# Performance work log

Hardware: AMD Instinct MI355X
Metric: run time of the kernel (lower is better)

Reference implementation:

```python
import jax, jax.numpy as jnp
import numpy as np

NUM_ITERATIONS = 3  # matches init kwarg num_iterations
B, R, CIN, COUT, K = 32, 2048, 64, 64, 16


def squash(s):
    # squash along the last (capsule-vector) axis, as in the torch module
    sq = jnp.sum(s * s, axis=-1, keepdims=True)
    return (sq / (1.0 + sq)) * s / jnp.sqrt(sq)


def setup_inputs() -> dict:
    key = jax.random.key(0)
    k1, k2 = jax.random.split(key)
    x = jax.random.normal(k1, (B, R, CIN), dtype=jnp.float32)
    route_weights = jax.random.normal(k2, (K, R, CIN, COUT), dtype=jnp.float32) * 0.05
    return {"x": x, "route_weights": route_weights}


def reference(x, route_weights):
    # priors[k,b,r,o] = sum_c x[b,r,c] * W[k,r,c,o]   -> [K, B, R, COUT]
    priors = jnp.einsum('brc,krco->kbro', x, route_weights)
    logits = jnp.zeros(priors.shape[:3] + (1,), dtype=priors.dtype)  # [K,B,R,1]
    outputs = None
    for i in range(NUM_ITERATIONS):
        probs = jax.nn.softmax(logits, axis=2)  # softmax over route nodes (torch dim=2)
        outputs = squash(jnp.sum(probs * priors, axis=2, keepdims=True))  # [K,B,1,COUT]
        if i != NUM_ITERATIONS - 1:
            logits = logits + jnp.sum(priors * outputs, axis=-1, keepdims=True)
    return outputs[:, :, 0, :]  # [K, B, COUT]
```

## Files before the change

### kernel.cpp

```cpp
#include <hip/hip_runtime.h>
#include <hip/hip_bf16.h>
#include <stdint.h>

#define NB 32
#define NR 2048
#define NC 64
#define NO 64
#define NK 16

using bf16x8 = __attribute__((ext_vector_type(8))) short;
using f32x4  = __attribute__((ext_vector_type(4))) float;

__device__ __forceinline__ uint32_t f2bf(float f) {
  uint32_t u = __builtin_bit_cast(uint32_t, f);
  return (u + 0x7fffu + ((u >> 16) & 1u)) >> 16;
}
__device__ __forceinline__ uint32_t packbf2(float lo, float hi) {
  return f2bf(lo) | (f2bf(hi) << 16);
}
__device__ __forceinline__ uint32_t cvtpk2(float lo, float hi) {
  float2 v; v.x = lo; v.y = hi;
  __hip_bfloat162 h = __float22bfloat162_rn(v);
  uint32_t r;
  __builtin_memcpy(&r, &h, 4);
  return r;
}

__global__ __launch_bounds__(256) void make_xbf(const float* __restrict__ x,
                                                ushort* __restrict__ xbf) {
  __shared__ float tile[32][72];
  const int r = blockIdx.x, t = threadIdx.x;
  {
    const int b = t >> 3, c0 = (t & 7) << 3;
    const float* xp = x + ((size_t)b * NR + r) * NC + c0;
    *(float4*)&tile[b][c0] = *(const float4*)xp;
    *(float4*)&tile[b][c0 + 4] = *(const float4*)(xp + 4);
  }
  __syncthreads();
  {
    const int ks = t >> 7, bt = (t >> 6) & 1, l = t & 63;
    const int kgrp = l >> 4;
    const int b = bt * 16 + (l & 15);
    const int cb = ks * 32 + kgrp;
    uint4 uv;
    uv.x = packbf2(tile[b][cb + 0], tile[b][cb + 4]);
    uv.y = packbf2(tile[b][cb + 8], tile[b][cb + 12]);
    uv.z = packbf2(tile[b][cb + 16], tile[b][cb + 20]);
    uv.w = packbf2(tile[b][cb + 24], tile[b][cb + 28]);
    *(uint4*)(xbf + (size_t)r * 2048 + t * 8) = uv;
  }
}

__global__ __launch_bounds__(256) void priors_gemm(const ushort* __restrict__ xbf,
                                                   const float* __restrict__ W,
                                                   ushort* __restrict__ priors) {
  __shared__ ushort ldsE[4][32 * 72];
  const int w = threadIdx.x >> 6, lane = threadIdx.x & 63;
  const int kgrp = lane >> 4, col = lane & 15;
  const int task = blockIdx.x * 4 + w;
  const int k = task & 15, r = task >> 4;
  const float* wbase = W + ((size_t)(k * NR + r)) * 4096;
  const ushort* xb = xbf + (size_t)r * 2048;

  bf16x8 xfrag[2][2];
#pragma unroll
  for (int ks = 0; ks < 2; ++ks)
#pragma unroll
    for (int bt = 0; bt < 2; ++bt)
      xfrag[ks][bt] = *(const bf16x8*)(xb + (ks * 2 + bt) * 512 + lane * 8);

  f32x4 acc[4][2];
#pragma unroll
  for (int ot = 0; ot < 4; ++ot)
#pragma unroll
    for (int bt = 0; bt < 2; ++bt) acc[ot][bt] = f32x4{0.f, 0.f, 0.f, 0.f};

#pragma unroll
  for (int ks = 0; ks < 2; ++ks) {
    float w32[4][8];
#pragma unroll
    for (int e = 0; e < 8; ++e) {
      const float* src = wbase + (ks * 32 + e * 4 + kgrp) * 64 + col;
#pragma unroll
      for (int ot = 0; ot < 4; ++ot) w32[ot][e] = src[ot * 16];
    }
#pragma unroll
    for (int ot = 0; ot < 4; ++ot) {
      uint4 uv;
      uv.x = cvtpk2(w32[ot][0], w32[ot][1]);
      uv.y = cvtpk2(w32[ot][2], w32[ot][3]);
      uv.z = cvtpk2(w32[ot][4], w32[ot][5]);
      uv.w = cvtpk2(w32[ot][6], w32[ot][7]);
      bf16x8 af = __builtin_bit_cast(bf16x8, uv);
      acc[ot][0] = __builtin_amdgcn_mfma_f32_16x16x32_bf16(af, xfrag[ks][0], acc[ot][0], 0, 0, 0);
      acc[ot][1] = __builtin_amdgcn_mfma_f32_16x16x32_bf16(af, xfrag[ks][1], acc[ot][1], 0, 0, 0);
    }
  }

  ushort* ep = &ldsE[w][0];
#pragma unroll
  for (int ot = 0; ot < 4; ++ot)
#pragma unroll
    for (int bt = 0; bt < 2; ++bt)
#pragma unroll
      for (int pr = 0; pr < 2; ++pr) {
        uint32_t u = cvtpk2(acc[ot][bt][pr * 2], acc[ot][bt][pr * 2 + 1]);
        const int b = bt * 16 + col, o = ot * 16 + kgrp * 4 + pr * 2;
        *(uint32_t*)(&ep[b * 72 + o]) = u;
      }
  ushort* pp = priors + ((size_t)(k * NR + r)) * 2048;
#pragma unroll
  for (int i = 0; i < 4; ++i) {
    const int row = (lane >> 3) + i * 8, cc = (lane & 7) * 8;
    uint4 v = *(const uint4*)(&ep[row * 72 + cc]);
    *(uint4*)(pp + row * 64 + cc) = v;
  }
}

template <int PASS>
__global__ __launch_bounds__(256) void routing(const __hip_bfloat16* __restrict__ priors,
                                               float* __restrict__ Abuf,
                                               const float* __restrict__ o_prev,
                                               float* __restrict__ o_out) {
  __shared__ float o_lds[64];
  __shared__ float red_num[4][8][8];
  __shared__ float red_den[4];
  const int kb = blockIdx.x;
  const int k = kb >> 5, b = kb & 31;
  const int tid = threadIdx.x, w = tid >> 6, lane = tid & 63;
  const int g = lane >> 3, sl = lane & 7;
  const int rsub = w * 8 + g;
  const __hip_bfloat16* pbase = priors + (size_t)k * NR * NB * NO + (size_t)b * NO;
  float* ab = Abuf + (size_t)kb * NR;

  if (PASS == 1) {
    float sum[8];
#pragma unroll
    for (int j = 0; j < 8; ++j) sum[j] = 0.f;
    for (int it = 0; it < NR / 32; ++it) {
      const int r = it * 32 + rsub;
      uint4 pv = *(const uint4*)(pbase + (size_t)r * (NB * NO) + sl * 8);
      sum[0] += __builtin_bit_cast(float, pv.x << 16);
      sum[1] += __builtin_bit_cast(float, pv.x & 0xffff0000u);
      sum[2] += __builtin_bit_cast(float, pv.y << 16);
      sum[3] += __builtin_bit_cast(float, pv.y & 0xffff0000u);
      sum[4] += __builtin_bit_cast(float, pv.z << 16);
      sum[5] += __builtin_bit_cast(float, pv.z & 0xffff0000u);
      sum[6] += __builtin_bit_cast(float, pv.w << 16);
      sum[7] += __builtin_bit_cast(float, pv.w & 0xffff0000u);
    }
#pragma unroll
    for (int m = 8; m < 64; m <<= 1)
#pragma unroll
      for (int j = 0; j < 8; ++j) sum[j] += __shfl_xor(sum[j], m, 64);
    if (lane < 8) {
#pragma unroll
      for (int j = 0; j < 8; ++j) red_num[w][lane][j] = sum[j];
    }
    __syncthreads();
    if (tid < 64) {
      const int s_ = tid >> 3, j_ = tid & 7;
      float sv = (red_num[0][s_][j_] + red_num[1][s_][j_] +
                  red_num[2][s_][j_] + red_num[3][s_][j_]) * (1.f / (float)NR);
      float sq = sv * sv;
#pragma unroll
      for (int m = 1; m < 64; m <<= 1) sq += __shfl_xor(sq, m, 64);
      o_lds[tid] = (sq / (1.f + sq)) * rsqrtf(sq) * sv;
    }
    __syncthreads();
  } else {
    if (tid < 64) o_lds[tid] = o_prev[kb * 64 + tid];
    __syncthreads();
  }

  float os[8];
#pragma unroll
  for (int j = 0; j < 8; ++j) os[j] = o_lds[sl * 8 + j];

  float num[8];
#pragma unroll
  for (int j = 0; j < 8; ++j) num[j] = 0.f;
  float den = 0.f;

  for (int it = 0; it < NR / 32; ++it) {
    const int r = it * 32 + rsub;
    uint4 pv = *(const uint4*)(pbase + (size_t)r * (NB * NO) + sl * 8);
    float f[8];
    f[0] = __builtin_bit_cast(float, pv.x << 16);
    f[1] = __builtin_bit_cast(float, pv.x & 0xffff0000u);
    f[2] = __builtin_bit_cast(float, pv.y << 16);
    f[3] = __builtin_bit_cast(float, pv.y & 0xffff0000u);
    f[4] = __builtin_bit_cast(float, pv.z << 16);
    f[5] = __builtin_bit_cast(float, pv.z & 0xffff0000u);
    f[6] = __builtin_bit_cast(float, pv.w << 16);
    f[7] = __builtin_bit_cast(float, pv.w & 0xffff0000u);

    float d = 0.f;
#pragma unroll
    for (int j = 0; j < 8; ++j) d = fmaf(f[j], os[j], d);
#pragma unroll
    for (int m = 1; m < 8; m <<= 1) d += __shfl_xor(d, m, 64);

    float lg;
    if (PASS == 1) {
      lg = d;
      if (sl == 0) ab[r] = d;
    } else {
      lg = d + ab[r];
    }
    float e = __expf(lg);
    den += e;
#pragma unroll
    for (int j = 0; j < 8; ++j) num[j] = fmaf(e, f[j], num[j]);
  }

#pragma unroll
  for (int m = 8; m < 64; m <<= 1) {
    den += __shfl_xor(den, m, 64);
#pragma unroll
    for (int j = 0; j < 8; ++j) num[j] += __shfl_xor(num[j], m, 64);
  }
  if (lane < 8) {
#pragma unroll
    for (int j = 0; j < 8; ++j) red_num[w][lane][j] = num[j];
    if (lane == 0) red_den[w] = den;
  }
  __syncthreads();

  if (tid < 64) {
    const int s_ = tid >> 3, j_ = tid & 7;
    float nm = red_num[0][s_][j_] + red_num[1][s_][j_] + red_num[2][s_][j_] + red_num[3][s_][j_];
    float dn = red_den[0] + red_den[1] + red_den[2] + red_den[3];
    float sv = nm / dn;
    float sq = sv * sv;
#pragma unroll
    for (int m = 1; m < 64; m <<= 1) sq += __shfl_xor(sq, m, 64);
    float ov = (sq / (1.f + sq)) * rsqrtf(sq) * sv;
    o_out[kb * 64 + tid] = ov;
  }
}

extern "C" void kernel_launch(void* const* d_in, const int* in_sizes, int n_in,
                              void* d_out, int out_size, void* d_ws, size_t ws_size,
                              hipStream_t stream) {
  const float* x = (const float*)d_in[0];
  const float* W = (const float*)d_in[1];
  float* out = (float*)d_out;
  char* ws = (char*)d_ws;

  size_t off = 0;
  ushort* xbf = (ushort*)(ws + off);               off += (size_t)NR * 2048 * 2;
  ushort* priors = (ushort*)(ws + off);            off += (size_t)NK * NR * NB * NO * 2;
  float* o1 = (float*)(ws + off);                  off += (size_t)NK * NB * NO * 4;
  float* Abuf = (float*)(ws + off);                off += (size_t)NK * NB * NR * 4;

  make_xbf<<<NR, 256, 0, stream>>>(x, xbf);
  priors_gemm<<<(NR * NK) / 4, 256, 0, stream>>>(xbf, W, priors);
  routing<1><<<NK * NB, 256, 0, stream>>>((const __hip_bfloat16*)priors, Abuf, nullptr, o1);
  routing<2><<<NK * NB, 256, 0, stream>>>((const __hip_bfloat16*)priors, Abuf, o1, out);
}
```

Baseline: 219.6 us.

## Fuse two routing passes into one kernel and hoist all W loads in GEMM

```diff
diff --git a/kernel.cpp b/kernel.cpp
--- a/kernel.cpp
+++ b/kernel.cpp
@@ -69,33 +69,35 @@
     for (int bt = 0; bt < 2; ++bt)
       xfrag[ks][bt] = *(const bf16x8*)(xb + (ks * 2 + bt) * 512 + lane * 8);
 
-  f32x4 acc[4][2];
-#pragma unroll
-  for (int ot = 0; ot < 4; ++ot)
-#pragma unroll
-    for (int bt = 0; bt < 2; ++bt) acc[ot][bt] = f32x4{0.f, 0.f, 0.f, 0.f};
-
-#pragma unroll
-  for (int ks = 0; ks < 2; ++ks) {
-    float w32[4][8];
+  float w32[2][4][8];
+#pragma unroll
+  for (int ks = 0; ks < 2; ++ks)
 #pragma unroll
     for (int e = 0; e < 8; ++e) {
       const float* src = wbase + (ks * 32 + e * 4 + kgrp) * 64 + col;
 #pragma unroll
-      for (int ot = 0; ot < 4; ++ot) w32[ot][e] = src[ot * 16];
-    }
+      for (int ot = 0; ot < 4; ++ot) w32[ks][ot][e] = src[ot * 16];
+    }
+
+  f32x4 acc[4][2];
+#pragma unroll
+  for (int ot = 0; ot < 4; ++ot)
+#pragma unroll
+    for (int bt = 0; bt < 2; ++bt) acc[ot][bt] = f32x4{0.f, 0.f, 0.f, 0.f};
+
+#pragma unroll
+  for (int ks = 0; ks < 2; ++ks)
 #pragma unroll
     for (int ot = 0; ot < 4; ++ot) {
       uint4 uv;
-      uv.x = cvtpk2(w32[ot][0], w32[ot][1]);
-      uv.y = cvtpk2(w32[ot][2], w32[ot][3]);
-      uv.z = cvtpk2(w32[ot][4], w32[ot][5]);
-      uv.w = cvtpk2(w32[ot][6], w32[ot][7]);
+      uv.x = cvtpk2(w32[ks][ot][0], w32[ks][ot][1]);
+      uv.y = cvtpk2(w32[ks][ot][2], w32[ks][ot][3]);
+      uv.z = cvtpk2(w32[ks][ot][4], w32[ks][ot][5]);
+      uv.w = cvtpk2(w32[ks][ot][6], w32[ks][ot][7]);
       bf16x8 af = __builtin_bit_cast(bf16x8, uv);
       acc[ot][0] = __builtin_amdgcn_mfma_f32_16x16x32_bf16(af, xfrag[ks][0], acc[ot][0], 0, 0, 0);
       acc[ot][1] = __builtin_amdgcn_mfma_f32_16x16x32_bf16(af, xfrag[ks][1], acc[ot][1], 0, 0, 0);
     }
-  }
 
   ushort* ep = &ldsE[w][0];
 #pragma unroll
@@ -117,23 +119,20 @@
   }
 }
 
-template <int PASS>
-__global__ __launch_bounds__(256) void routing(const __hip_bfloat16* __restrict__ priors,
-                                               float* __restrict__ Abuf,
-                                               const float* __restrict__ o_prev,
-                                               float* __restrict__ o_out) {
+__global__ __launch_bounds__(256) void routing_fused(const __hip_bfloat16* __restrict__ priors,
+                                                     float* __restrict__ o_out) {
   __shared__ float o_lds[64];
   __shared__ float red_num[4][8][8];
   __shared__ float red_den[4];
+  __shared__ float ar[2048];
   const int kb = blockIdx.x;
   const int k = kb >> 5, b = kb & 31;
   const int tid = threadIdx.x, w = tid >> 6, lane = tid & 63;
   const int g = lane >> 3, sl = lane & 7;
   const int rsub = w * 8 + g;
   const __hip_bfloat16* pbase = priors + (size_t)k * NR * NB * NO + (size_t)b * NO;
-  float* ab = Abuf + (size_t)kb * NR;
-
-  if (PASS == 1) {
+
+  {
     float sum[8];
 #pragma unroll
     for (int j = 0; j < 8; ++j) sum[j] = 0.f;
@@ -168,75 +167,77 @@
       o_lds[tid] = (sq / (1.f + sq)) * rsqrtf(sq) * sv;
     }
     __syncthreads();
-  } else {
-    if (tid < 64) o_lds[tid] = o_prev[kb * 64 + tid];
-    __syncthreads();
-  }
-
-  float os[8];
-#pragma unroll
-  for (int j = 0; j < 8; ++j) os[j] = o_lds[sl * 8 + j];
-
-  float num[8];
-#pragma unroll
-  for (int j = 0; j < 8; ++j) num[j] = 0.f;
-  float den = 0.f;
-
-  for (int it = 0; it < NR / 32; ++it) {
-    const int r = it * 32 + rsub;
-    uint4 pv = *(const uint4*)(pbase + (size_t)r * (NB * NO) + sl * 8);
-    float f[8];
-    f[0] = __builtin_bit_cast(float, pv.x << 16);
-    f[1] = __builtin_bit_cast(float, pv.x & 0xffff0000u);
-    f[2] = __builtin_bit_cast(float, pv.y << 16);
-    f[3] = __builtin_bit_cast(float, pv.y & 0xffff0000u);
-    f[4] = __builtin_bit_cast(float, pv.z << 16);
-    f[5] = __builtin_bit_cast(float, pv.z & 0xffff0000u);
-    f[6] = __builtin_bit_cast(float, pv.w << 16);
-    f[7] = __builtin_bit_cast(float, pv.w & 0xffff0000u);
-
-    float d = 0.f;
-#pragma unroll
-    for (int j = 0; j < 8; ++j) d = fmaf(f[j], os[j], d);
-#pragma unroll
-    for (int m = 1; m < 8; m <<= 1) d += __shfl_xor(d, m, 64);
-
-    float lg;
-    if (PASS == 1) {
-      lg = d;
-      if (sl == 0) ab[r] = d;
-    } else {
-      lg = d + ab[r];
-    }
-    float e = __expf(lg);
-    den += e;
-#pragma unroll
-    for (int j = 0; j < 8; ++j) num[j] = fmaf(e, f[j], num[j]);
-  }
-
-#pragma unroll
-  for (int m = 8; m < 64; m <<= 1) {
-    den += __shfl_xor(den, m, 64);
-#pragma unroll
-    for (int j = 0; j < 8; ++j) num[j] += __shfl_xor(num[j], m, 64);
-  }
-  if (lane < 8) {
-#pragma unroll
-    for (int j = 0; j < 8; ++j) red_num[w][lane][j] = num[j];
-    if (lane == 0) red_den[w] = den;
-  }
-  __syncthreads();
-
-  if (tid < 64) {
-    const int s_ = tid >> 3, j_ = tid & 7;
-    float nm = red_num[0][s_][j_] + red_num[1][s_][j_] + red_num[2][s_][j_] + red_num[3][s_][j_];
-    float dn = red_den[0] + red_den[1] + red_den[2] + red_den[3];
-    float sv = nm / dn;
-    float sq = sv * sv;
-#pragma unroll
-    for (int m = 1; m < 64; m <<= 1) sq += __shfl_xor(sq, m, 64);
-    float ov = (sq / (1.f + sq)) * rsqrtf(sq) * sv;
-    o_out[kb * 64 + tid] = ov;
+  }
+
+#pragma unroll 1
+  for (int pass = 0; pass < 2; ++pass) {
+    float os[8];
+#pragma unroll
+    for (int j = 0; j < 8; ++j) os[j] = o_lds[sl * 8 + j];
+
+    float num[8];
+#pragma unroll
+    for (int j = 0; j < 8; ++j) num[j] = 0.f;
+    float den = 0.f;
+
+    for (int it = 0; it < NR / 32; ++it) {
+      const int r = it * 32 + rsub;
+      uint4 pv = *(const uint4*)(pbase + (size_t)r * (NB * NO) + sl * 8);
+      float f[8];
+      f[0] = __builtin_bit_cast(float, pv.x << 16);
+      f[1] = __builtin_bit_cast(float, pv.x & 0xffff0000u);
+      f[2] = __builtin_bit_cast(float, pv.y << 16);
+      f[3] = __builtin_bit_cast(float, pv.y & 0xffff0000u);
+      f[4] = __builtin_bit_cast(float, pv.z << 16);
+      f[5] = __builtin_bit_cast(float, pv.z & 0xffff0000u);
+      f[6] = __builtin_bit_cast(float, pv.w << 16);
+      f[7] = __builtin_bit_cast(float, pv.w & 0xffff0000u);
+
+      float d = 0.f;
+#pragma unroll
+      for (int j = 0; j < 8; ++j) d = fmaf(f[j], os[j], d);
+#pragma unroll
+      for (int m = 1; m < 8; m <<= 1) d += __shfl_xor(d, m, 64);
+
+      float lg;
+      if (pass == 0) {
+        lg = d;
+        if (sl == 0) ar[r] = d;
+      } else {
+        lg = d + ar[r];
+      }
+      float e = __expf(lg);
+      den += e;
+#pragma unroll
+      for (int j = 0; j < 8; ++j) num[j] = fmaf(e, f[j], num[j]);
+    }
+
+#pragma unroll
+    for (int m = 8; m < 64; m <<= 1) {
+      den += __shfl_xor(den, m, 64);
+#pragma unroll
+      for (int j = 0; j < 8; ++j) num[j] += __shfl_xor(num[j], m, 64);
+    }
+    if (lane < 8) {
+#pragma unroll
+      for (int j = 0; j < 8; ++j) red_num[w][lane][j] = num[j];
+      if (lane == 0) red_den[w] = den;
+    }
+    __syncthreads();
+
+    if (tid < 64) {
+      const int s_ = tid >> 3, j_ = tid & 7;
+      float nm = red_num[0][s_][j_] + red_num[1][s_][j_] + red_num[2][s_][j_] + red_num[3][s_][j_];
+      float dn = red_den[0] + red_den[1] + red_den[2] + red_den[3];
+      float sv = nm / dn;
+      float sq = sv * sv;
+#pragma unroll
+      for (int m = 1; m < 64; m <<= 1) sq += __shfl_xor(sq, m, 64);
+      float ov = (sq / (1.f + sq)) * rsqrtf(sq) * sv;
+      if (pass == 0) o_lds[tid] = ov;
+      else           o_out[kb * 64 + tid] = ov;
+    }
+    __syncthreads();
   }
 }
 
@@ -251,11 +252,8 @@
   size_t off = 0;
   ushort* xbf = (ushort*)(ws + off);               off += (size_t)NR * 2048 * 2;
   ushort* priors = (ushort*)(ws + off);            off += (size_t)NK * NR * NB * NO * 2;
-  float* o1 = (float*)(ws + off);                  off += (size_t)NK * NB * NO * 4;
-  float* Abuf = (float*)(ws + off);                off += (size_t)NK * NB * NR * 4;
 
   make_xbf<<<NR, 256, 0, stream>>>(x, xbf);
   priors_gemm<<<(NR * NK) / 4, 256, 0, stream>>>(xbf, W, priors);
-  routing<1><<<NK * NB, 256, 0, stream>>>((const __hip_bfloat16*)priors, Abuf, nullptr, o1);
-  routing<2><<<NK * NB, 256, 0, stream>>>((const __hip_bfloat16*)priors, Abuf, o1, out);
-}
+  routing_fused<<<NK * NB, 256, 0, stream>>>((const __hip_bfloat16*)priors, out);
+}
```

Result: slower. 231.7 us (+5.5%).
